# Optimization experiments

Hardware: AMD Instinct MI355X
Metric: run time of the kernel (lower is better)

The kernel has to match this reference:

```python
import jax, jax.numpy as jnp
import numpy as np
from jax import lax

WSIZE = 11
SIGMA = 1.5
PAD = WSIZE // 2  # 5
C1 = 0.01 ** 2
C2 = 0.03 ** 2


def _gauss1d():
    x = np.arange(WSIZE) - WSIZE // 2
    g = np.exp(-(x.astype(np.float64) ** 2) / (2.0 * SIGMA ** 2))
    g = g / g.sum()
    return jnp.asarray(g, dtype=jnp.float32)


def _blur3d(x, g):
    """Replicate-pad by 5 on D/H/W then apply the separable 11x11x11 Gaussian.
    x: [N, 1, D, H, W]. Mathematically identical to the dense conv3d in the
    original (the 3D window is an exact outer product of the 1D Gaussian)."""
    xp = jnp.pad(x, ((0, 0), (0, 0), (PAD, PAD), (PAD, PAD), (PAD, PAD)), mode='edge')
    dn = ('NCDHW', 'OIDHW', 'NCDHW')
    for kshape in ((1, 1, WSIZE, 1, 1), (1, 1, 1, WSIZE, 1), (1, 1, 1, 1, WSIZE)):
        xp = lax.conv_general_dilated(xp, g.reshape(kshape), (1, 1, 1), 'VALID',
                                      dimension_numbers=dn)
    return xp


def _rerange(img):
    img = jnp.where(img.max() > 128.0, img / 255.0, img)
    img = jnp.where(img.min() < -0.5, (img + 1.0) / 2.0, img)
    return img


def setup_inputs() -> dict:
    key = jax.random.key(0)
    k1, k2 = jax.random.split(key)
    N, C, H, W = 4, 16, 512, 512
    pred = jax.random.uniform(k1, (N, C, H, W), dtype=jnp.float32)
    gt = jax.random.uniform(k2, (N, C, H, W), dtype=jnp.float32)
    return {"pred": pred, "gt": gt}


def reference(pred, gt):
    N = pred.shape[0]
    pred = _rerange(pred)
    gt = _rerange(gt)

    # ---- PSNR (range = 1.0, reduce='sum') ----
    mse = jnp.mean((pred - gt) ** 2, axis=(1, 2, 3))           # [N]
    psnr = jnp.sum(10.0 * jnp.log10(1.0 / mse))                # scalar

    # ---- 3D SSIM over [N,1,C,H,W] volumes ----
    g = _gauss1d()
    img = pred[:, None]                                        # [N,1,D,H,W]
    gtt = gt[:, None]
    mu1 = _blur3d(img, g)
    mu2 = _blur3d(gtt, g)
    mu1_sq = mu1 * mu1
    mu2_sq = mu2 * mu2
    mu1_mu2 = mu1 * mu2
    sigma1_sq = _blur3d(img * img, g) - mu1_sq
    sigma2_sq = _blur3d(gtt * gtt, g) - mu2_sq
    sigma12 = _blur3d(img * gtt, g) - mu1_mu2

    v1 = 2.0 * sigma12 + C2
    v2 = sigma1_sq + sigma2_sq + C2
    ssim_map = ((2.0 * mu1_mu2 + C1) * v1) / ((mu1_sq + mu2_sq + C1) * v2)
    ssim = jnp.sum(jnp.mean(ssim_map, axis=(1, 2, 3, 4)))      # reduce='sum'

    return psnr, ssim, N
```

## Files before the change

### kernel.cpp

```cpp
#include <hip/hip_runtime.h>
#include <cmath>


#define NB 4
#define DD 16
#define HH 512
#define WW 512
#define SLICE (HH * WW)
#define VOL (DD * SLICE)
#define C1F 0.0001f
#define C2F 0.0009f

#define TH 16
#define TW 16
#define SCOLS 26
#define NRP 13
#define PW 14
#define PLSTR 28
#define SDW (NRP * PLSTR)
#define TMW (TH * PW)
#define NTHR 256
#define SIT (NRP * SCOLS)
#define XTRA (SIT - NTHR)
#define HITEMS 104

typedef _Float16 h2v __attribute__((ext_vector_type(2)));

struct KArg {
  unsigned ge[6], go[6];
  float wlT[DD * DD];
};

__device__ inline float dot2h(unsigned a, unsigned b, float c) {
#if __has_builtin(__builtin_amdgcn_fdot2)
  return __builtin_amdgcn_fdot2(__builtin_bit_cast(h2v, a),
                                __builtin_bit_cast(h2v, b), c, false);
#else
  h2v av = __builtin_bit_cast(h2v, a), bv = __builtin_bit_cast(h2v, b);
  return fmaf((float)av.y, (float)bv.y, fmaf((float)av.x, (float)bv.x, c));
#endif
}
__device__ inline unsigned pkh(float a, float b) {
  return __builtin_bit_cast(unsigned, __builtin_amdgcn_cvt_pkrtz(a, b));
}
__device__ inline int iclamp(int v, int lo, int hi) {
  return v < lo ? lo : (v > hi ? hi : v);
}

__device__ inline float block_sum256(float v) {
#pragma unroll
  for (int o = 32; o > 0; o >>= 1) v += __shfl_down(v, o, 64);
  __shared__ float r[4];
  if ((threadIdx.x & 63) == 0) r[threadIdx.x >> 6] = v;
  __syncthreads();
  float out = 0.f;
  if (threadIdx.x == 0) {
#pragma unroll
    for (int i = 0; i < 4; ++i) out += r[i];
  }
  __syncthreads();
  return out;
}

__global__ void zero_acc_k(float* acc) {
  if (threadIdx.x < 8) acc[threadIdx.x] = 0.f;
}

__global__ __launch_bounds__(NTHR, 3) void fused_k(
    const float* __restrict__ pred, const float* __restrict__ gt,
    float* __restrict__ acc, KArg ka) {
  __shared__ uint4 sd[SDW];
  __shared__ uint4 tmp[TMW];

  int b0 = blockIdx.x;
  int b = (b0 & 7) * ((NB * 1024) >> 3) + (b0 >> 3);
  int tile = b & 1023;
  int n = b >> 10;
  int th0 = (tile >> 5) * TH;
  int tw0 = (tile & 31) * TW;
  int t = threadIdx.x;

  int rp0 = t / SCOLS, x0 = t - rp0 * SCOLS;
  int gx0 = iclamp(tw0 + x0 - 5, 0, WW - 1);
  int go0a = iclamp(th0 + 2 * rp0 - 5, 0, HH - 1) * WW + gx0;
  int go0b = iclamp(th0 + 2 * rp0 - 4, 0, HH - 1) * WW + gx0;
  int w0i = (2 * rp0 + (x0 & 1)) * PW + (x0 >> 1);
  bool ox0 = (x0 >= 5) && (x0 < 5 + TW);
  float o0a = (ox0 && rp0 >= 3 && rp0 <= 10) ? 1.f : 0.f;
  float o0b = (ox0 && rp0 >= 2 && rp0 <= 9) ? 1.f : 0.f;
  int i1 = t + XTRA;
  bool has2 = (i1 >= NTHR);
  int rp1 = i1 / SCOLS, x1 = i1 - rp1 * SCOLS;
  int gx1 = iclamp(tw0 + x1 - 5, 0, WW - 1);
  int go1a = iclamp(th0 + 2 * rp1 - 5, 0, HH - 1) * WW + gx1;
  int go1b = iclamp(th0 + 2 * rp1 - 4, 0, HH - 1) * WW + gx1;
  int w1i = (2 * rp1 + (x1 & 1)) * PW + (x1 >> 1);
  bool ox1 = (x1 >= 5) && (x1 < 5 + TW);
  float o1a = (ox1 && rp1 >= 3 && rp1 <= 10) ? 1.f : 0.f;
  float o1b = (ox1 && rp1 >= 2 && rp1 <= 9) ? 1.f : 0.f;

  bool hasH = (t < HITEMS);
  int hm = t & 7, hcp = t >> 3;
  int hrd = hm * PLSTR + hcp;
  int hwr = (2 * hm) * PW + hcp;

  int wx = t & 15;
  int wrd = (t >> 4) * PW + (wx >> 1);
  unsigned cw[6];
#pragma unroll
  for (int J = 0; J < 6; ++J) cw[J] = (wx & 1) ? ka.go[J] : ka.ge[J];

  const float* pb = pred + (size_t)n * VOL;
  const float* qb = gt + (size_t)n * VOL;

  float p0a = pb[go0a], p0b = pb[go0b], q0a = qb[go0a], q0b = qb[go0b];
  float p1a = 0.f, p1b = 0.f, q1a = 0.f, q1b = 0.f;
  if (has2) { p1a = pb[go1a]; p1b = pb[go1b]; q1a = qb[go1a]; q1b = qb[go1b]; }

  float psnr = 0.f;
  float a0[DD], a1[DD], a2[DD], a3[DD];
#pragma unroll
  for (int j = 0; j < DD; ++j) { a0[j] = a1[j] = a2[j] = a3[j] = 0.f; }

#pragma unroll 1
  for (int d = 0; d < DD; ++d) {
    {
      float SA = p0a + q0a, DA = p0a - q0a;
      float SB = p0b + q0b, DB = p0b - q0b;
      float dA = DA * DA, dB = DB * DB;
      psnr = fmaf(o0a, dA, psnr);
      psnr = fmaf(o0b, dB, psnr);
      sd[w0i] = make_uint4(pkh(SA, SB), pkh(DA, DB),
                           pkh(SA * SA, SB * SB), pkh(dA, dB));
    }
    if (has2) {
      float SA = p1a + q1a, DA = p1a - q1a;
      float SB = p1b + q1b, DB = p1b - q1b;
      float dA = DA * DA, dB = DB * DB;
      psnr = fmaf(o1a, dA, psnr);
      psnr = fmaf(o1b, dB, psnr);
      sd[w1i] = make_uint4(pkh(SA, SB), pkh(DA, DB),
                           pkh(SA * SA, SB * SB), pkh(dA, dB));
    }
    __syncthreads();

    if (d < DD - 1) {
      const float* P = pb + (size_t)(d + 1) * SLICE;
      const float* Q = qb + (size_t)(d + 1) * SLICE;
      p0a = P[go0a]; p0b = P[go0b]; q0a = Q[go0a]; q0b = Q[go0b];
      if (has2) { p1a = P[go1a]; p1b = P[go1b]; q1a = Q[go1a]; q1b = Q[go1b]; }
    }

    if (hasH) {
      float e0[4] = {0, 0, 0, 0}, e1[4] = {0, 0, 0, 0};
      float r0[4] = {0, 0, 0, 0}, r1[4] = {0, 0, 0, 0};
#pragma unroll
      for (int J = 0; J < 6; ++J) {
        uint4 ve = sd[hrd + J * PLSTR];
        uint4 vo = sd[hrd + J * PLSTR + PW];
        unsigned cge = ka.ge[J], cgo = ka.go[J];
        e0[0] = dot2h(cge, ve.x, e0[0]); e0[1] = dot2h(cge, ve.y, e0[1]);
        e0[2] = dot2h(cge, ve.z, e0[2]); e0[3] = dot2h(cge, ve.w, e0[3]);
        r0[0] = dot2h(cgo, ve.x, r0[0]); r0[1] = dot2h(cgo, ve.y, r0[1]);
        r0[2] = dot2h(cgo, ve.z, r0[2]); r0[3] = dot2h(cgo, ve.w, r0[3]);
        e1[0] = dot2h(cge, vo.x, e1[0]); e1[1] = dot2h(cge, vo.y, e1[1]);
        e1[2] = dot2h(cge, vo.z, e1[2]); e1[3] = dot2h(cge, vo.w, e1[3]);
        r1[0] = dot2h(cgo, vo.x, r1[0]); r1[1] = dot2h(cgo, vo.y, r1[1]);
        r1[2] = dot2h(cgo, vo.z, r1[2]); r1[3] = dot2h(cgo, vo.w, r1[3]);
      }
      tmp[hwr] = make_uint4(pkh(e0[0], e1[0]), pkh(e0[1], e1[1]),
                            pkh(e0[2], e1[2]), pkh(e0[3], e1[3]));
      tmp[hwr + PW] = make_uint4(pkh(r0[0], r1[0]), pkh(r0[1], r1[1]),
                                 pkh(r0[2], r1[2]), pkh(r0[3], r1[3]));
    }
    __syncthreads();

    float w0 = 0.f, w1 = 0.f, w2 = 0.f, w3 = 0.f;
#pragma unroll
    for (int J = 0; J < 6; ++J) {
      uint4 v = tmp[wrd + J];
      w0 = dot2h(cw[J], v.x, w0); w1 = dot2h(cw[J], v.y, w1);
      w2 = dot2h(cw[J], v.z, w2); w3 = dot2h(cw[J], v.w, w3);
    }
    const float* wl = ka.wlT + d * DD;
#pragma unroll
    for (int o = 0; o < DD; ++o) {
      float w = wl[o];
      a0[o] = fmaf(w, w0, a0[o]);
      a1[o] = fmaf(w, w1, a1[o]);
      a2[o] = fmaf(w, w2, a2[o]);
      a3[o] = fmaf(w, w3, a3[o]);
    }
  }

  float ssum = 0.f;
#pragma unroll
  for (int j = 0; j < DD; ++j) {
    float Sb = a0[j], Db = a1[j], B1 = a2[j], B2 = a3[j];
    float SS = Sb * Sb, DDm = Db * Db;
    float m12_2 = (SS - DDm) * 0.5f;
    float msq   = (SS + DDm) * 0.5f;
    float Epq   = (B1 - B2) * 0.25f;
    float Esum  = (B1 + B2) * 0.5f;
    float sig12_2 = 2.f * Epq - m12_2;
    float svar    = Esum - msq;
    float num = (m12_2 + C1F) * (sig12_2 + C2F);
    float den = (msq + C1F) * (svar + C2F);
    ssum += num / den;
  }
  float bs = block_sum256(ssum);
  if (t == 0) atomicAdd(&acc[4 + n], bs);
  float bp = block_sum256(psnr);
  if (t == 0) atomicAdd(&acc[n], bp);
}

__global__ void final_k(const float* __restrict__ acc, float* __restrict__ out) {
  if (threadIdx.x == 0 && blockIdx.x == 0) {
    double psnr = 0.0, ssim = 0.0;
    for (int n = 0; n < NB; ++n) {
      double mse = (double)acc[n] / (double)VOL;
      psnr += 10.0 * log10(1.0 / mse);
      ssim += (double)acc[4 + n] / (double)VOL;
    }
    out[0] = (float)psnr;
    out[1] = (float)ssim;
    out[2] = (float)NB;
  }
}

static unsigned short f2h(float f) {
  union { float f; unsigned u; } v; v.f = f;
  unsigned u = v.u;
  unsigned s = (u >> 16) & 0x8000u;
  int e = (int)((u >> 23) & 0xff) - 127 + 15;
  unsigned m = u & 0x7fffffu;
  if (e <= 0) return (unsigned short)s;
  if (e >= 31) return (unsigned short)(s | 0x7c00u);
  unsigned h = ((unsigned)e << 10) | (m >> 13);
  unsigned rem = m & 0x1fffu;
  if (rem > 0x1000u || (rem == 0x1000u && (h & 1u))) h++;
  return (unsigned short)(s | h);
}
static float h2f(unsigned short h) {
  unsigned se = (h >> 10) & 0x1f, m = h & 0x3ffu, s = ((unsigned)h & 0x8000u) << 16;
  union { unsigned u; float f; } v;
  if (se == 0) { v.u = s; return v.f; }
  v.u = s | ((se - 15 + 127) << 23) | (m << 13);
  return v.f;
}

extern "C" void kernel_launch(void* const* d_in, const int* in_sizes, int n_in,
                              void* d_out, int out_size, void* d_ws, size_t ws_size,
                              hipStream_t stream) {
  const float* pred = (const float*)d_in[0];
  const float* gt = (const float*)d_in[1];
  float* acc = (float*)d_ws;

  double tt[11], s = 0.0;
  for (int i = 0; i < 11; ++i) {
    double x = i - 5;
    tt[i] = exp(-(x * x) / 4.5);
    s += tt[i];
  }
  float g[11];
  for (int i = 0; i < 11; ++i) g[i] = (float)(tt[i] / s);

  unsigned short hg[11];
  for (int i = 0; i < 11; ++i) hg[i] = f2h(g[i]);
  for (int pass = 0; pass < 3; ++pass) {
    double sum = 0.0;
    for (int i = 0; i < 11; ++i) sum += (double)h2f(hg[i]);
    hg[5] = f2h((float)((double)h2f(hg[5]) + (1.0 - sum)));
  }

  KArg ka;
  for (int j = 0; j < 5; ++j)
    ka.ge[j] = (unsigned)hg[2 * j] | ((unsigned)hg[2 * j + 1] << 16);
  ka.ge[5] = (unsigned)hg[10];
  ka.go[0] = ((unsigned)hg[0]) << 16;
  for (int j = 1; j < 6; ++j)
    ka.go[j] = (unsigned)hg[2 * j - 1] | ((unsigned)hg[2 * j] << 16);

  for (int o = 0; o < DD; ++o)
    for (int d = 0; d < DD; ++d) {
      float w = 0.f;
      for (int k = 0; k < 11; ++k) {
        int j = o + k - 5;
        j = j < 0 ? 0 : (j > 15 ? 15 : j);
        if (j == d) w += g[k];
      }
      ka.wlT[d * DD + o] = w;
    }

  zero_acc_k<<<1, 64, 0, stream>>>(acc);
  fused_k<<<NB * 1024, NTHR, 0, stream>>>(pred, gt, acc, ka);
  final_k<<<1, 1, 0, stream>>>(acc, (float*)d_out);
}
```

Before: 252.4 us.

## Move depth blur to MFMA matrix multiply with fp16 staging in LDS

The per-thread 16-tap depth accumulation in fp32 registers (64 accumulators per thread, one FMA per tap) is replaced. The W-blurred slices are now packed as fp16 into a 32 KB LDS staging buffer, and after the depth loop a 16x16x32 fp16 MFMA applies the depth weight matrix. The W pass now runs on half the threads, each producing both even and odd outputs. The intent is to cut register pressure and VALU work. In exchange it adds LDS footprint that may lower occupancy, adds fp16 rounding of intermediates and weights, and leaves some MFMA lanes doing zero padding work.

Result: slower. 262.3 us (+3.9%).

```diff
diff --git a/kernel.cpp b/kernel.cpp
--- a/kernel.cpp
+++ b/kernel.cpp
@@ -25,10 +25,12 @@
 #define HITEMS 104
 
 typedef _Float16 h2v __attribute__((ext_vector_type(2)));
+typedef _Float16 h8 __attribute__((ext_vector_type(8)));
+typedef float f4 __attribute__((ext_vector_type(4)));
 
 struct KArg {
   unsigned ge[6], go[6];
-  float wlT[DD * DD];
+  unsigned wlf[256];
 };
 
 __device__ inline float dot2h(unsigned a, unsigned b, float c) {
@@ -40,6 +42,10 @@
   return fmaf((float)av.y, (float)bv.y, fmaf((float)av.x, (float)bv.x, c));
 #endif
 }
+__device__ inline f4 mfma16(uint4 a, uint4 b, f4 c) {
+  return __builtin_amdgcn_mfma_f32_16x16x32_f16(
+      __builtin_bit_cast(h8, a), __builtin_bit_cast(h8, b), c, 0, 0, 0);
+}
 __device__ inline unsigned pkh(float a, float b) {
   return __builtin_bit_cast(unsigned, __builtin_amdgcn_cvt_pkrtz(a, b));
 }
@@ -71,6 +77,8 @@
     float* __restrict__ acc, KArg ka) {
   __shared__ uint4 sd[SDW];
   __shared__ uint4 tmp[TMW];
+  __shared__ _Float16 ost[4 * 256 * 16];
+  __shared__ uint4 zzq;
 
   int b0 = blockIdx.x;
   int b = (b0 & 7) * ((NB * 1024) >> 3) + (b0 >> 3);
@@ -79,6 +87,10 @@
   int th0 = (tile >> 5) * TH;
   int tw0 = (tile & 31) * TW;
   int t = threadIdx.x;
+  int lane = t & 63, wv = t >> 6;
+  int lo = lane & 15, hi = lane >> 4;
+
+  if (t == 0) zzq = make_uint4(0, 0, 0, 0);
 
   int rp0 = t / SCOLS, x0 = t - rp0 * SCOLS;
   int gx0 = iclamp(tw0 + x0 - 5, 0, WW - 1);
@@ -104,11 +116,13 @@
   int hrd = hm * PLSTR + hcp;
   int hwr = (2 * hm) * PW + hcp;
 
-  int wx = t & 15;
-  int wrd = (t >> 4) * PW + (wx >> 1);
-  unsigned cw[6];
-#pragma unroll
-  for (int J = 0; J < 6; ++J) cw[J] = (wx & 1) ? ka.go[J] : ka.ge[J];
+  bool hasW = (t >= 128);
+  int u = (t - 128) & 127;
+  int wy = u >> 3, wxh = u & 7;
+  int wrd = wy * PW + wxh;
+  int px0 = wy * 16 + 2 * wxh;
+  int qx = 2 * ((wy >> 2) & 1);
+  int owb0 = px0 * 4;
 
   const float* pb = pred + (size_t)n * VOL;
   const float* qb = gt + (size_t)n * VOL;
@@ -118,9 +132,11 @@
   if (has2) { p1a = pb[go1a]; p1b = pb[go1b]; q1a = qb[go1a]; q1b = qb[go1b]; }
 
   float psnr = 0.f;
-  float a0[DD], a1[DD], a2[DD], a3[DD];
-#pragma unroll
-  for (int j = 0; j < DD; ++j) { a0[j] = a1[j] = a2[j] = a3[j] = 0.f; }
+  float se0 = 0, se1 = 0, se2 = 0, se3 = 0, so0 = 0, so1 = 0, so2 = 0, so3 = 0;
+  unsigned pAe0 = 0, pAe1 = 0, pAe2 = 0, pAe3 = 0;
+  unsigned pAo0 = 0, pAo1 = 0, pAo2 = 0, pAo3 = 0;
+
+  __syncthreads();
 
 #pragma unroll 1
   for (int d = 0; d < DD; ++d) {
@@ -175,38 +191,75 @@
     }
     __syncthreads();
 
-    float w0 = 0.f, w1 = 0.f, w2 = 0.f, w3 = 0.f;
-#pragma unroll
-    for (int J = 0; J < 6; ++J) {
-      uint4 v = tmp[wrd + J];
-      w0 = dot2h(cw[J], v.x, w0); w1 = dot2h(cw[J], v.y, w1);
-      w2 = dot2h(cw[J], v.z, w2); w3 = dot2h(cw[J], v.w, w3);
-    }
-    const float* wl = ka.wlT + d * DD;
-#pragma unroll
-    for (int o = 0; o < DD; ++o) {
-      float w = wl[o];
-      a0[o] = fmaf(w, w0, a0[o]);
-      a1[o] = fmaf(w, w1, a1[o]);
-      a2[o] = fmaf(w, w2, a2[o]);
-      a3[o] = fmaf(w, w3, a3[o]);
-    }
-  }
-
+    if (hasW) {
+      float e0 = 0, e1 = 0, e2 = 0, e3 = 0;
+      float o0 = 0, o1 = 0, o2 = 0, o3 = 0;
+#pragma unroll
+      for (int J = 0; J < 6; ++J) {
+        uint4 v = tmp[wrd + J];
+        unsigned cE = ka.ge[J], cO = ka.go[J];
+        e0 = dot2h(cE, v.x, e0); e1 = dot2h(cE, v.y, e1);
+        e2 = dot2h(cE, v.z, e2); e3 = dot2h(cE, v.w, e3);
+        o0 = dot2h(cO, v.x, o0); o1 = dot2h(cO, v.y, o1);
+        o2 = dot2h(cO, v.z, o2); o3 = dot2h(cO, v.w, o3);
+      }
+      if ((d & 1) == 0) {
+        se0 = e0; se1 = e1; se2 = e2; se3 = e3;
+        so0 = o0; so1 = o1; so2 = o2; so3 = o3;
+      } else if ((d & 2) == 0) {
+        pAe0 = pkh(se0, e0); pAe1 = pkh(se1, e1);
+        pAe2 = pkh(se2, e2); pAe3 = pkh(se3, e3);
+        pAo0 = pkh(so0, o0); pAo1 = pkh(so1, o1);
+        pAo2 = pkh(so2, o2); pAo3 = pkh(so3, o3);
+      } else {
+        int Qp = (d >> 2) ^ qx;
+        uint2* op = (uint2*)ost;
+        op[owb0 + Qp]        = make_uint2(pAe0, pkh(se0, e0));
+        op[owb0 + 1024 + Qp] = make_uint2(pAe1, pkh(se1, e1));
+        op[owb0 + 2048 + Qp] = make_uint2(pAe2, pkh(se2, e2));
+        op[owb0 + 3072 + Qp] = make_uint2(pAe3, pkh(se3, e3));
+        op[owb0 + 4 + Qp]        = make_uint2(pAo0, pkh(so0, o0));
+        op[owb0 + 4 + 1024 + Qp] = make_uint2(pAo1, pkh(so1, o1));
+        op[owb0 + 4 + 2048 + Qp] = make_uint2(pAo2, pkh(so2, o2));
+        op[owb0 + 4 + 3072 + Qp] = make_uint2(pAo3, pkh(so3, o3));
+      }
+    }
+  }
+  __syncthreads();
+
+  uint4 wlf = ((const uint4*)ka.wlf)[lane];
+  const uint4* oq = (const uint4*)ost;
+  f4 z4 = {0.f, 0.f, 0.f, 0.f};
+  int bnt = wv & 1;
+  int blk = (hi < 2) ? (hi ^ bnt) : 0;
+  bool real = (hi < 2);
   float ssum = 0.f;
 #pragma unroll
-  for (int j = 0; j < DD; ++j) {
-    float Sb = a0[j], Db = a1[j], B1 = a2[j], B2 = a3[j];
-    float SS = Sb * Sb, DDm = Db * Db;
-    float m12_2 = (SS - DDm) * 0.5f;
-    float msq   = (SS + DDm) * 0.5f;
-    float Epq   = (B1 - B2) * 0.25f;
-    float Esum  = (B1 + B2) * 0.5f;
-    float sig12_2 = 2.f * Epq - m12_2;
-    float svar    = Esum - msq;
-    float num = (m12_2 + C1F) * (sig12_2 + C2F);
-    float den = (msq + C1F) * (svar + C2F);
-    ssum += num / den;
+  for (int q = 0; q < 4; ++q) {
+    int nt = 4 * wv + q;
+    int bidx = (16 * nt + lo) * 2 + blk;
+    const uint4* bp0 = real ? &oq[bidx] : &zzq;
+    const uint4* bp1 = real ? &oq[512 + bidx] : &zzq;
+    const uint4* bp2 = real ? &oq[1024 + bidx] : &zzq;
+    const uint4* bp3 = real ? &oq[1536 + bidx] : &zzq;
+    f4 cS = mfma16(wlf, *bp0, z4);
+    f4 cD = mfma16(wlf, *bp1, z4);
+    f4 cS2 = mfma16(wlf, *bp2, z4);
+    f4 cD2 = mfma16(wlf, *bp3, z4);
+#pragma unroll
+    for (int r = 0; r < 4; ++r) {
+      float Sb = cS[r], Db = cD[r], B1 = cS2[r], B2 = cD2[r];
+      float SS = Sb * Sb, DDm = Db * Db;
+      float m12_2 = (SS - DDm) * 0.5f;
+      float msq = (SS + DDm) * 0.5f;
+      float Epq = (B1 - B2) * 0.25f;
+      float Esum = (B1 + B2) * 0.5f;
+      float sig12_2 = 2.f * Epq - m12_2;
+      float svar = Esum - msq;
+      float num = (m12_2 + C1F) * (sig12_2 + C2F);
+      float den = (msq + C1F) * (svar + C2F);
+      ssum += num / den;
+    }
   }
   float bs = block_sum256(ssum);
   if (t == 0) atomicAdd(&acc[4 + n], bs);
@@ -281,6 +334,7 @@
   for (int j = 1; j < 6; ++j)
     ka.go[j] = (unsigned)hg[2 * j - 1] | ((unsigned)hg[2 * j] << 16);
 
+  float wl[DD][DD];
   for (int o = 0; o < DD; ++o)
     for (int d = 0; d < DD; ++d) {
       float w = 0.f;
@@ -289,8 +343,29 @@
         j = j < 0 ? 0 : (j > 15 ? 15 : j);
         if (j == d) w += g[k];
       }
-      ka.wlT[d * DD + o] = w;
-    }
+      wl[d][o] = w;
+    }
+  unsigned short wlh[DD][DD];
+  for (int o = 0; o < DD; ++o) {
+    int dmx = 0;
+    for (int d = 0; d < DD; ++d) {
+      wlh[o][d] = f2h(wl[d][o]);
+      if (wl[d][o] > wl[dmx][o]) dmx = d;
+    }
+    for (int pass = 0; pass < 3; ++pass) {
+      double sum = 0.0;
+      for (int d = 0; d < DD; ++d) sum += (double)h2f(wlh[o][d]);
+      wlh[o][dmx] = f2h((float)((double)h2f(wlh[o][dmx]) + (1.0 - sum)));
+    }
+  }
+  for (int l = 0; l < 64; ++l) {
+    int lo = l & 15, hi = l >> 4;
+    unsigned short v[8];
+    for (int i = 0; i < 8; ++i)
+      v[i] = (hi < 2) ? wlh[lo][8 * hi + i] : 0;
+    for (int k = 0; k < 4; ++k)
+      ka.wlf[l * 4 + k] = (unsigned)v[2 * k] | ((unsigned)v[2 * k + 1] << 16);
+  }
 
   zero_acc_k<<<1, 64, 0, stream>>>(acc);
   fused_k<<<NB * 1024, NTHR, 0, stream>>>(pred, gt, acc, ka);
```
